# Optimization experiments

Measured on AMD Instinct MI355X. Metric: run time of the kernel, lower is better.

Reference implementation:

```python
import jax, jax.numpy as jnp
import numpy as np

# dims
A, T, K, H, NH, F, L = 64, 50, 6, 128, 8, 60, 512
M = A * T * K          # 19200 mode nodes (layout: agent, time, mode)
AT = A * T             # 3200 agent-timestep nodes
NL = 10                # GA layers: t2m,l2m,m2m_h,m2m_a,m2m_s,t2n,l2n,n2n_h,n2n_a,n2n_s
FF = 4 * H
E = 150000


def _ln(x, g, b):
    mu = x.mean(-1, keepdims=True)
    var = jnp.mean((x - mu) ** 2, axis=-1, keepdims=True)
    return (x - mu) * jax.lax.rsqrt(var + 1e-5) * g + b


def _mlp(x, W1, b1, W2, b2):
    return jax.nn.relu(x @ W1 + b1) @ W2 + b2


def _edge_emb(attr, i, eW1, eb1, eW2, eb2):
    # pad raw edge features to width 5 so all embed MLPs share a stacked param layout
    x = jnp.pad(attr, ((0, 0), (0, 5 - attr.shape[-1])))
    return jax.nn.relu(x @ eW1[i] + eb1[i]) @ eW2[i] + eb2[i]


def _segment_softmax(scores, dst, n):
    smax = jax.ops.segment_max(scores, dst, num_segments=n)
    smax = jnp.where(jnp.isfinite(smax), smax, 0.0)
    ex = jnp.exp(scores - smax[dst])
    den = jax.ops.segment_sum(ex, dst, num_segments=n)
    return ex / (den[dst] + 1e-9)


def _graph_attention(i, x_src, x_dst, ei, edge_emb, p):
    (Wq, Wk, Wv, Wo, Wke, Wve, g1, b1, g2, b2, fW1, fb1, fW2, fb2) = p
    src, dst = ei[0], ei[1]
    dh = H // NH
    n_dst = x_dst.shape[0]
    xd = _ln(x_dst, g1[i], b1[i])
    xs = _ln(x_src, g1[i], b1[i])
    q = (xd @ Wq[i]).reshape(n_dst, NH, dh)
    k = (xs @ Wk[i])[src]            # gather per-edge keys  [E,H]
    v = (xs @ Wv[i])[src]
    if edge_emb is not None:
        k = k + edge_emb @ Wke[i]
        v = v + edge_emb @ Wve[i]
    k = k.reshape(-1, NH, dh)
    v = v.reshape(-1, NH, dh)
    scores = jnp.sum(q[dst] * k, axis=-1) / np.sqrt(dh)   # [E,NH]
    attn = _segment_softmax(scores, dst, n_dst)
    agg = jax.ops.segment_sum(attn[..., None] * v, dst, num_segments=n_dst)
    x = x_dst + agg.reshape(n_dst, H) @ Wo[i]
    h = _ln(x, g2[i], b2[i])
    return x + _mlp(h, fW1[i], fb1[i], fW2[i], fb2[i])


def _forward(a_input, l_embs, mode_tokens,
             emb_W1, emb_b1, emb_W2, emb_b2,
             ga_Wq, ga_Wk, ga_Wv, ga_Wo, ga_Wke, ga_Wve,
             ga_g1, ga_b1, ga_g2, ga_b2, ga_fW1, ga_fb1, ga_fW2, ga_fb2,
             tp_W1, tp_b1, tp_W2, tp_b2,
             pa_W1, pa_b1, pa_W2, pa_b2,
             tr_W1, tr_b1, tr_W2, tr_b2,
             t2m_attr, l2m_attr, m2m_h_attr, m2m_a_attr,
             t2m_ei, l2m_ei, m2m_h_ei, m2m_a_ei, m2m_s_ei):
    ga = (ga_Wq, ga_Wk, ga_Wv, ga_Wo, ga_Wke, ga_Wve,
          ga_g1, ga_b1, ga_g2, ga_b2, ga_fW1, ga_fb1, ga_fW2, ga_fb2)
    # agent embedding: TwoLayerMLP on [vel_len, vel_theta, length, width, type]
    a_embs = (jax.nn.relu(a_input @ emb_W1[0] + emb_b1[0]) @ emb_W2[0] + emb_b2[0]).reshape(AT, H)
    # mode tokens broadcast over (agent, time)
    m = jnp.broadcast_to(mode_tokens, (A, T, K, H)).reshape(M, H)
    # edge-attr embeddings (gather-compute pattern)
    t2m_e = _edge_emb(t2m_attr, 1, emb_W1, emb_b1, emb_W2, emb_b2)
    l2m_e = _edge_emb(l2m_attr, 2, emb_W1, emb_b1, emb_W2, emb_b2)
    m2m_h_e = _edge_emb(m2m_h_attr, 3, emb_W1, emb_b1, emb_W2, emb_b2)
    m2m_a_e = _edge_emb(m2m_a_attr, 4, emb_W1, emb_b1, emb_W2, emb_b2)
    # proposal stage
    m = _graph_attention(0, a_embs, m, t2m_ei, t2m_e, ga)
    m = _graph_attention(1, l_embs, m, l2m_ei, l2m_e, ga)
    m = _graph_attention(2, m, m, m2m_h_ei, m2m_h_e, ga)
    m = _graph_attention(3, m, m, m2m_a_ei, m2m_a_e, ga)
    m = _graph_attention(4, m, m, m2m_s_ei, None, ga)
    m_last = m.reshape(A, T, K, H)[:, -1]                 # [A,K,H]
    proposal = _mlp(m_last, tp_W1, tp_b1, tp_W2, tp_b2)   # [A,K,2F]
    anchor = _mlp(proposal, pa_W1, pa_b1, pa_W2, pa_b2)   # [A,K,H]
    # refinement stage on anchor-conditioned mode nodes
    n = (m.reshape(A, T, K, H) + anchor[:, None]).reshape(M, H)
    n = _graph_attention(5, a_embs, n, t2m_ei, t2m_e, ga)
    n = _graph_attention(6, l_embs, n, l2m_ei, l2m_e, ga)
    n = _graph_attention(7, n, n, m2m_h_ei, m2m_h_e, ga)
    n = _graph_attention(8, n, n, m2m_a_ei, m2m_a_e, ga)
    n = _graph_attention(9, n, n, m2m_s_ei, None, ga)
    n_last = n.reshape(A, T, K, H)[:, -1]
    refine = proposal + _mlp(n_last, tr_W1, tr_b1, tr_W2, tr_b2)
    return jnp.stack([proposal, refine])                  # [2,A,K,2F]


def setup_inputs() -> dict:
    key = jax.random.key(0)
    ks = list(jax.random.split(key, 64))
    it = iter(ks)
    nx = lambda: next(it)
    p = lambda *s: 0.02 * jax.random.normal(nx(), s, dtype=jnp.float32)
    inp = {}
    inp['a_input'] = jax.random.normal(nx(), (A, T, 5), dtype=jnp.float32)
    inp['l_embs'] = jax.random.normal(nx(), (L, H), dtype=jnp.float32)
    inp['mode_tokens'] = p(K, H)
    # stacked edge/feature embed MLPs: 0:a,1:t2m,2:l2m,3:m2m_h,4:m2m_a
    inp['emb_W1'] = p(5, 5, H); inp['emb_b1'] = jnp.zeros((5, H), jnp.float32)
    inp['emb_W2'] = p(5, H, H); inp['emb_b2'] = jnp.zeros((5, H), jnp.float32)
    # stacked GraphAttention params
    for nm in ['ga_Wq', 'ga_Wk', 'ga_Wv', 'ga_Wo', 'ga_Wke', 'ga_Wve']:
        inp[nm] = p(NL, H, H)
    inp['ga_g1'] = jnp.ones((NL, H), jnp.float32); inp['ga_b1'] = jnp.zeros((NL, H), jnp.float32)
    inp['ga_g2'] = jnp.ones((NL, H), jnp.float32); inp['ga_b2'] = jnp.zeros((NL, H), jnp.float32)
    inp['ga_fW1'] = p(NL, H, FF); inp['ga_fb1'] = jnp.zeros((NL, FF), jnp.float32)
    inp['ga_fW2'] = p(NL, FF, H); inp['ga_fb2'] = jnp.zeros((NL, H), jnp.float32)
    # heads
    inp['tp_W1'] = p(H, H); inp['tp_b1'] = jnp.zeros((H,), jnp.float32)
    inp['tp_W2'] = p(H, 2 * F); inp['tp_b2'] = jnp.zeros((2 * F,), jnp.float32)
    inp['pa_W1'] = p(2 * F, H); inp['pa_b1'] = jnp.zeros((H,), jnp.float32)
    inp['pa_W2'] = p(H, H); inp['pa_b2'] = jnp.zeros((H,), jnp.float32)
    inp['tr_W1'] = p(H, H); inp['tr_b1'] = jnp.zeros((H,), jnp.float32)
    inp['tr_W2'] = p(H, 2 * F); inp['tr_b2'] = jnp.zeros((2 * F,), jnp.float32)
    # raw edge features
    inp['t2m_attr'] = jax.random.normal(nx(), (E, 4), dtype=jnp.float32)
    inp['l2m_attr'] = jax.random.normal(nx(), (E, 3), dtype=jnp.float32)
    inp['m2m_h_attr'] = jax.random.normal(nx(), (E, 4), dtype=jnp.float32)
    inp['m2m_a_attr'] = jax.random.normal(nx(), (E, 3), dtype=jnp.float32)
    # edge indices (src row range differs per graph)
    ri = lambda hi: jax.random.randint(nx(), (E,), 0, hi, dtype=jnp.int32)
    inp['t2m_ei'] = jnp.stack([ri(AT), ri(M)])
    inp['l2m_ei'] = jnp.stack([ri(L), ri(M)])
    inp['m2m_h_ei'] = jnp.stack([ri(M), ri(M)])
    inp['m2m_a_ei'] = jnp.stack([ri(M), ri(M)])
    inp['m2m_s_ei'] = jnp.stack([ri(M), ri(M)])
    return inp


def reference(a_input, l_embs, mode_tokens,
              emb_W1, emb_b1, emb_W2, emb_b2,
              ga_Wq, ga_Wk, ga_Wv, ga_Wo, ga_Wke, ga_Wve,
              ga_g1, ga_b1, ga_g2, ga_b2, ga_fW1, ga_fb1, ga_fW2, ga_fb2,
              tp_W1, tp_b1, tp_W2, tp_b2,
              pa_W1, pa_b1, pa_W2, pa_b2,
              tr_W1, tr_b1, tr_W2, tr_b2,
              t2m_attr, l2m_attr, m2m_h_attr, m2m_a_attr,
              t2m_ei, l2m_ei, m2m_h_ei, m2m_a_ei, m2m_s_ei):
    return _forward(a_input, l_embs, mode_tokens,
                    emb_W1, emb_b1, emb_W2, emb_b2,
                    ga_Wq, ga_Wk, ga_Wv, ga_Wo, ga_Wke, ga_Wve,
                    ga_g1, ga_b1, ga_g2, ga_b2, ga_fW1, ga_fb1, ga_fW2, ga_fb2,
                    tp_W1, tp_b1, tp_W2, tp_b2,
                    pa_W1, pa_b1, pa_W2, pa_b2,
                    tr_W1, tr_b1, tr_W2, tr_b2,
                    t2m_attr, l2m_attr, m2m_h_attr, m2m_a_attr,
                    t2m_ei, l2m_ei, m2m_h_ei, m2m_a_ei, m2m_s_ei)
```

## Files before the change

kernel.cpp:

```cpp
#include <hip/hip_runtime.h>
#include <hip/hip_bf16.h>
#include <math.h>

#define DEV __device__ __forceinline__

typedef __attribute__((ext_vector_type(4))) float floatx4;
typedef __attribute__((ext_vector_type(8))) __bf16 bf16x8;

static constexpr int A_ = 64, T_ = 50, K_ = 6, H_ = 128, NH_ = 8, F_ = 60, L_ = 512;
static constexpr int M_  = A_ * T_ * K_;
static constexpr int AT_ = A_ * T_;
static constexpr int FF_ = 4 * H_;
static constexpr int NL_ = 10;
static constexpr int P2F = 2 * F_;
static constexpr int AK_ = A_ * K_;
static constexpr size_t WLAY = 196608;

DEV ushort f2bh(float f) {
    unsigned u = __float_as_uint(f);
    unsigned r = u + 0x7FFFu + ((u >> 16) & 1u);
    return (ushort)(r >> 16);
}
DEV float bh2f(ushort h) { return __uint_as_float(((unsigned)h) << 16); }

__global__ __launch_bounds__(256) void ln_kernel(const float* __restrict__ x,
                                                 const float* __restrict__ g,
                                                 const float* __restrict__ b,
                                                 float* __restrict__ y, int n) {
    int row = blockIdx.x * 4 + (threadIdx.x >> 6);
    int lane = threadIdx.x & 63;
    if (row >= n) return;
    const float* xr = x + (size_t)row * H_;
    float v0 = xr[lane], v1 = xr[lane + 64];
    float s = v0 + v1;
    for (int m = 32; m >= 1; m >>= 1) s += __shfl_xor(s, m, 64);
    float mu = s * (1.f / 128.f);
    float d0 = v0 - mu, d1 = v1 - mu;
    float vs = d0 * d0 + d1 * d1;
    for (int m = 32; m >= 1; m >>= 1) vs += __shfl_xor(vs, m, 64);
    float rs = rsqrtf(vs * (1.f / 128.f) + 1e-5f);
    float* yr = y + (size_t)row * H_;
    yr[lane]      = d0 * rs * g[lane] + b[lane];
    yr[lane + 64] = d1 * rs * g[lane + 64] + b[lane + 64];
}

template <int ACT, bool RES>
__global__ __launch_bounds__(256) void mgemm(const float* __restrict__ X,
                                             const ushort* __restrict__ Wh,
                                             const ushort* __restrict__ Wl,
                                             const float* __restrict__ bias,
                                             const float* __restrict__ res,
                                             float* __restrict__ Y,
                                             int n, int Kd, int C) {
    __shared__ ushort lds[4 * 8192];
    ushort* Xh  = lds;
    ushort* Xl  = lds + 8192;
    ushort* Wsh = lds + 16384;
    ushort* Wsl = lds + 24576;
    int row0 = blockIdx.x * 128, col0 = blockIdx.y * 128;
    int tid = threadIdx.x;
    int lane = tid & 63, wid = tid >> 6;
    int rbase = (wid >> 1) * 64, cbase = (wid & 1) * 64;
    int lrow = lane & 15, lk = lane >> 4;
    floatx4 acc[4][4];
#pragma unroll
    for (int a = 0; a < 4; a++)
#pragma unroll
        for (int b2 = 0; b2 < 4; b2++) acc[a][b2] = floatx4{0.f, 0.f, 0.f, 0.f};

    for (int k0 = 0; k0 < Kd; k0 += 64) {
#pragma unroll
        for (int i = 0; i < 8; i++) {
            int idx = tid + i * 256;
            int r = idx >> 4, kc = idx & 15;
            float4 v = *(const float4*)(X + (size_t)(row0 + r) * Kd + k0 + kc * 4);
            ushort h0 = f2bh(v.x), h1 = f2bh(v.y), h2 = f2bh(v.z), h3 = f2bh(v.w);
            ushort l0 = f2bh(v.x - bh2f(h0)), l1 = f2bh(v.y - bh2f(h1)),
                   l2 = f2bh(v.z - bh2f(h2)), l3 = f2bh(v.w - bh2f(h3));
            int base = (r << 6) + (((kc >> 1) ^ (r & 7)) << 3) + ((kc & 1) << 2);
            *(ushort4*)(Xh + base) = make_ushort4(h0, h1, h2, h3);
            *(ushort4*)(Xl + base) = make_ushort4(l0, l1, l2, l3);
        }
#pragma unroll
        for (int i = 0; i < 4; i++) {
            int idx = tid + i * 256;
            int c = idx >> 3, ch = idx & 7;
            int base = (c << 6) + ((ch ^ (c & 7)) << 3);
            size_t go = (size_t)(col0 + c) * Kd + k0 + ch * 8;
            *(float4*)(Wsh + base) = *(const float4*)(Wh + go);
            *(float4*)(Wsl + base) = *(const float4*)(Wl + go);
        }
        __syncthreads();
#pragma unroll
        for (int kk = 0; kk < 2; kk++) {
            int ch = kk * 4 + lk;
            bf16x8 xh[4], xl[4], wh[4], wl[4];
#pragma unroll
            for (int s = 0; s < 4; s++) {
                int r = rbase + s * 16 + lrow;
                int xoff = (r << 6) + ((ch ^ (r & 7)) << 3);
                xh[s] = *(const bf16x8*)(Xh + xoff);
                xl[s] = *(const bf16x8*)(Xl + xoff);
                int c = cbase + s * 16 + lrow;
                int woff = (c << 6) + ((ch ^ (c & 7)) << 3);
                wh[s] = *(const bf16x8*)(Wsh + woff);
                wl[s] = *(const bf16x8*)(Wsl + woff);
            }
#pragma unroll
            for (int sr = 0; sr < 4; sr++)
#pragma unroll
                for (int sc = 0; sc < 4; sc++) {
                    acc[sr][sc] = __builtin_amdgcn_mfma_f32_16x16x32_bf16(wh[sc], xh[sr], acc[sr][sc], 0, 0, 0);
                    acc[sr][sc] = __builtin_amdgcn_mfma_f32_16x16x32_bf16(wl[sc], xh[sr], acc[sr][sc], 0, 0, 0);
                    acc[sr][sc] = __builtin_amdgcn_mfma_f32_16x16x32_bf16(wh[sc], xl[sr], acc[sr][sc], 0, 0, 0);
                }
        }
        __syncthreads();
    }
#pragma unroll
    for (int sr = 0; sr < 4; sr++) {
        int row = row0 + rbase + sr * 16 + lrow;
#pragma unroll
        for (int sc = 0; sc < 4; sc++) {
            int col = col0 + cbase + sc * 16 + lk * 4;
            size_t o = (size_t)row * C + col;
            float4 v = make_float4(acc[sr][sc][0], acc[sr][sc][1],
                                   acc[sr][sc][2], acc[sr][sc][3]);
            if (bias) { float4 bv = *(const float4*)(bias + col);
                        v.x += bv.x; v.y += bv.y; v.z += bv.z; v.w += bv.w; }
            if (ACT == 1) { v.x = fmaxf(v.x, 0.f); v.y = fmaxf(v.y, 0.f);
                            v.z = fmaxf(v.z, 0.f); v.w = fmaxf(v.w, 0.f); }
            if (RES) { float4 rv = *(const float4*)(res + o);
                       v.x += rv.x; v.y += rv.y; v.z += rv.z; v.w += rv.w; }
            *(float4*)(Y + o) = v;
        }
    }
}

__global__ __launch_bounds__(256) void prep_w(const float* __restrict__ Wq,
                                              const float* __restrict__ Wk,
                                              const float* __restrict__ Wv,
                                              const float* __restrict__ Wo,
                                              const float* __restrict__ fW1,
                                              const float* __restrict__ fW2,
                                              ushort* __restrict__ oh,
                                              ushort* __restrict__ ol) {
    int l = blockIdx.y, t = blockIdx.x;
    const float* src; int K, C, tiles_c; size_t obase;
    if (t < 64) {
        int mi = t >> 4; t &= 15;
        src = (mi == 0 ? Wq : mi == 1 ? Wk : mi == 2 ? Wv : Wo) + (size_t)l * 16384;
        K = 128; C = 128; tiles_c = 4; obase = (size_t)l * WLAY + (size_t)mi * 16384;
    } else if (t < 128) {
        t -= 64; src = fW1 + (size_t)l * 65536;
        K = 128; C = 512; tiles_c = 16; obase = (size_t)l * WLAY + 65536;
    } else {
        t -= 128; src = fW2 + (size_t)l * 65536;
        K = 512; C = 128; tiles_c = 4; obase = (size_t)l * WLAY + 131072;
    }
    int tc = t % tiles_c, tk = t / tiles_c;
    __shared__ float tile[32][33];
    int tx = threadIdx.x & 31, ty = threadIdx.x >> 5;
#pragma unroll
    for (int i = 0; i < 4; i++) {
        int k = tk * 32 + ty + i * 8;
        tile[ty + i * 8][tx] = src[(size_t)k * C + tc * 32 + tx];
    }
    __syncthreads();
#pragma unroll
    for (int i = 0; i < 4; i++) {
        int c = tc * 32 + ty + i * 8;
        float v = tile[tx][ty + i * 8];
        ushort h = f2bh(v);
        ushort lo = f2bh(v - bh2f(h));
        size_t o = obase + (size_t)c * K + tk * 32 + tx;
        oh[o] = h; ol[o] = lo;
    }
}

template <int ACT, bool RES>
__global__ void small_gemm(const float* __restrict__ X, const float* __restrict__ W,
                           const float* __restrict__ bias, const float* __restrict__ res,
                           float* __restrict__ Y, int n, int Kd, int C) {
    int idx = blockIdx.x * 256 + threadIdx.x;
    if (idx >= n * C) return;
    int row = idx / C, c = idx - row * C;
    float a = bias ? bias[c] : 0.f;
    const float* xr = X + (size_t)row * Kd;
    for (int k = 0; k < Kd; k++) a = fmaf(xr[k], W[(size_t)k * C + c], a);
    if (ACT == 1) a = fmaxf(a, 0.f);
    if (RES) a += res[idx];
    Y[idx] = a;
}

__global__ __launch_bounds__(256) void combine_fast(const float* __restrict__ eW2,
                                                    const float* __restrict__ Wke,
                                                    const float* __restrict__ Wve,
                                                    float* __restrict__ cW) {
    __shared__ float Xs[128 * 36];
    __shared__ float Ws[32 * 128];
    int x = blockIdx.x;
    int li = x & 7, kv = x >> 3;
    int l = li < 4 ? li : li + 1;
    int g = (li & 3) + 1;
    const float* E2 = eW2 + (size_t)g * 16384;
    const float* Wp = (kv ? Wve : Wke) + (size_t)l * 16384;
    float* out = cW + (size_t)l * 32768 + kv * 128;
    int tid = threadIdx.x;
    int tc = tid & 15, tr = tid >> 4;
    int cA = tc * 4, rA = tr * 4;
    float acc[8][8] = {};
    for (int j0 = 0; j0 < 128; j0 += 32) {
#pragma unroll
        for (int i = 0; i < 4; i++) {
            int idx = tid + i * 256;
            int r = idx >> 3, jc = idx & 7;
            *(float4*)(Xs + r * 36 + jc * 4) =
                *(const float4*)(E2 + (size_t)r * 128 + j0 + jc * 4);
        }
#pragma unroll
        for (int i = 0; i < 4; i++) {
            int idx = tid + i * 256;
            int cc = idx & 31, jj = idx >> 5;
            *(float4*)(Ws + jj * 128 + cc * 4) =
                *(const float4*)(Wp + (size_t)(j0 + jj) * 128 + cc * 4);
        }
        __syncthreads();
#pragma unroll 8
        for (int jj = 0; jj < 32; jj++) {
            float4 w0 = *(const float4*)(Ws + jj * 128 + cA);
            float4 w1 = *(const float4*)(Ws + jj * 128 + cA + 64);
            float xr[8];
#pragma unroll
            for (int i2 = 0; i2 < 4; i2++) {
                xr[i2]     = Xs[(rA + i2) * 36 + jj];
                xr[4 + i2] = Xs[(rA + i2 + 64) * 36 + jj];
            }
#pragma unroll
            for (int i2 = 0; i2 < 8; i2++) {
                float xv = xr[i2];
                acc[i2][0] = fmaf(xv, w0.x, acc[i2][0]);
                acc[i2][1] = fmaf(xv, w0.y, acc[i2][1]);
                acc[i2][2] = fmaf(xv, w0.z, acc[i2][2]);
                acc[i2][3] = fmaf(xv, w0.w, acc[i2][3]);
                acc[i2][4] = fmaf(xv, w1.x, acc[i2][4]);
                acc[i2][5] = fmaf(xv, w1.y, acc[i2][5]);
                acc[i2][6] = fmaf(xv, w1.z, acc[i2][6]);
                acc[i2][7] = fmaf(xv, w1.w, acc[i2][7]);
            }
        }
        __syncthreads();
    }
#pragma unroll
    for (int i = 0; i < 8; i++) {
        int r = (i < 4) ? (rA + i) : (rA + i + 60);
#pragma unroll
        for (int chh = 0; chh < 2; chh++) {
            int c = cA + chh * 64;
            *(float4*)(out + (size_t)r * 256 + c) =
                make_float4(acc[i][chh * 4 + 0], acc[i][chh * 4 + 1],
                            acc[i][chh * 4 + 2], acc[i][chh * 4 + 3]);
        }
    }
}
__global__ void combine_bias(const float* __restrict__ eb2,
                             const float* __restrict__ Wke,
                             const float* __restrict__ Wve,
                             float* __restrict__ cb) {
    int x = blockIdx.x;
    int li = x & 7, kv = x >> 3;
    int l = li < 4 ? li : li + 1;
    int g = (li & 3) + 1;
    const float* Wp = (kv ? Wve : Wke) + (size_t)l * 16384;
    const float* eb = eb2 + g * 128;
    int cc = threadIdx.x;
    float a = 0.f;
    for (int j = 0; j < 128; j++) a = fmaf(eb[j], Wp[(size_t)j * 128 + cc], a);
    cb[l * 256 + kv * 128 + cc] = a;
}

__global__ void zero_i32(int* __restrict__ p, int n) {
    int i = blockIdx.x * 256 + threadIdx.x;
    if (i < n) p[i] = 0;
}
__global__ void hist_kernel(const int* __restrict__ dst, int E, int* __restrict__ deg) {
    int e = blockIdx.x * 256 + threadIdx.x;
    if (e < E) atomicAdd(&deg[dst[e]], 1);
}
__global__ __launch_bounds__(256) void exscan5(const int* __restrict__ deg0,
                                               int* __restrict__ off0,
                                               int* __restrict__ cursor0, int n) {
    int g = blockIdx.x;
    const int* deg = deg0 + (size_t)g * n;
    int* off = off0 + (size_t)g * (n + 1);
    int* cursor = cursor0 + (size_t)g * n;
    __shared__ int wsum[4];
    __shared__ int carry;
    int tid = threadIdx.x, lane = tid & 63, w = tid >> 6;
    if (tid == 0) carry = 0;
    __syncthreads();
    for (int base = 0; base < n; base += 256) {
        int v = (base + tid < n) ? deg[base + tid] : 0;
        int incl = v;
        for (int d = 1; d < 64; d <<= 1) {
            int t = __shfl_up(incl, d, 64);
            if (lane >= d) incl += t;
        }
        if (lane == 63) wsum[w] = incl;
        __syncthreads();
        int woff = 0;
        for (int i = 0; i < w; i++) woff += wsum[i];
        int total = wsum[0] + wsum[1] + wsum[2] + wsum[3];
        int excl = carry + woff + incl - v;
        if (base + tid < n) { off[base + tid] = excl; cursor[base + tid] = excl; }
        __syncthreads();
        if (tid == 0) carry += total;
        __syncthreads();
    }
    if (threadIdx.x == 0) off[n] = carry;
}
__global__ void scatter_kernel(const int* __restrict__ dst, int E,
                               int* __restrict__ cursor, int* __restrict__ eids) {
    int e = blockIdx.x * 256 + threadIdx.x;
    if (e < E) { int p = atomicAdd(&cursor[dst[e]], 1); eids[p] = e; }
}
__global__ void sort_edges(const int* __restrict__ eid, const int* __restrict__ srcArr,
                           const float* __restrict__ attr, int aw, int E,
                           int* __restrict__ esrc, float4* __restrict__ eattr) {
    int pos = blockIdx.x * 256 + threadIdx.x;
    if (pos >= E) return;
    int e = eid[pos];
    esrc[pos] = srcArr[e];
    if (attr) {
        float4 v;
        v.x = attr[(size_t)e * aw + 0];
        v.y = attr[(size_t)e * aw + 1];
        v.z = (aw > 2) ? attr[(size_t)e * aw + 2] : 0.f;
        v.w = (aw > 3) ? attr[(size_t)e * aw + 3] : 0.f;
        eattr[pos] = v;
    }
}

__global__ __launch_bounds__(256) void prep_g(const float* __restrict__ q,
                                              const float* __restrict__ cWl,
                                              const float* __restrict__ cbl,
                                              ushort* __restrict__ g,
                                              float* __restrict__ sb) {
    __shared__ float qs[8 * 132];
    int tid = threadIdx.x;
    int cp = tid & 127, hb = (tid >> 7) * 4;
    float ck[64];
    {
        const float* csrc = cWl + (size_t)cp * 256 + hb * 16;
#pragma unroll
        for (int t4 = 0; t4 < 16; t4++) {
            float4 v = *(const float4*)(csrc + t4 * 4);
            ck[t4 * 4 + 0] = v.x; ck[t4 * 4 + 1] = v.y;
            ck[t4 * 4 + 2] = v.z; ck[t4 * 4 + 3] = v.w;
        }
    }
    int d0 = blockIdx.x * 8;
    {
        int dl = tid >> 5, col = (tid & 31) * 4;
        *(float4*)(qs + dl * 132 + col) = *(const float4*)(q + (size_t)(d0 + dl) * 128 + col);
    }
    __syncthreads();
#pragma unroll
    for (int dl = 0; dl < 8; dl++) {
        const float* qr = qs + dl * 132 + hb * 16;
        float a0 = 0.f, a1 = 0.f, a2 = 0.f, a3 = 0.f;
#pragma unroll
        for (int t = 0; t < 16; t++) {
            a0 = fmaf(ck[t],      qr[t],      a0);
            a1 = fmaf(ck[16 + t], qr[16 + t], a1);
            a2 = fmaf(ck[32 + t], qr[32 + t], a2);
            a3 = fmaf(ck[48 + t], qr[48 + t], a3);
        }
        ushort4 o = make_ushort4(f2bh(a0 * 0.25f), f2bh(a1 * 0.25f),
                                 f2bh(a2 * 0.25f), f2bh(a3 * 0.25f));
        *(ushort4*)(g + (size_t)(d0 + dl) * 1024 + cp * 8 + hb) = o;
    }
    if (tid < 64) {
        int dl = tid >> 3, h = tid & 7;
        const float* qr = qs + dl * 132 + h * 16;
        const float* cbr = cbl + h * 16;
        float a = 0.f;
#pragma unroll
        for (int t = 0; t < 16; t++) a = fmaf(cbr[t], qr[t], a);
        sb[(d0 + dl) * 8 + h] = a * 0.25f;
    }
}

__global__ __launch_bounds__(256) void attn_fact(const int* __restrict__ off,
                                                 const int* __restrict__ esrc,
                                                 const float4* __restrict__ eattr,
                                                 const ushort* __restrict__ g,
                                                 const float* __restrict__ sb,
                                                 const float* __restrict__ eW1,
                                                 const float* __restrict__ eb1,
                                                 const float* __restrict__ kx,
                                                 const float* __restrict__ vx,
                                                 const float* __restrict__ q,
                                                 ushort* __restrict__ hsum,
                                                 float* __restrict__ vxacc,
                                                 float* __restrict__ den) {
    __shared__ float lds[4 * 144];
    int w = threadIdx.x >> 6, l = threadIdx.x & 63;
    int i = l & 15, hlo = l >> 4;
    float* hw = lds + w * 144;
    int d = blockIdx.x * 4 + w;
    int beg = off[d], end = off[d + 1];
    float q0 = q[(size_t)d * 128 + l] * 0.25f;
    float q1 = q[(size_t)d * 128 + 64 + l] * 0.25f;
    float gA[8], gB[8];
#pragma unroll
    for (int j = 0; j < 8; j++) {
        gA[j] = bh2f(g[(size_t)d * 1024 + (j * 16 + i) * 8 + hlo]);
        gB[j] = bh2f(g[(size_t)d * 1024 + (j * 16 + i) * 8 + hlo + 4]);
    }
    float sbA = sb[d * 8 + hlo], sbB = sb[d * 8 + 4 + hlo];
    float w1a[4], w1b[4];
#pragma unroll
    for (int j = 0; j < 4; j++) { w1a[j] = eW1[j * 128 + l]; w1b[j] = eW1[j * 128 + 64 + l]; }
    float ebA = eb1[l], ebB = eb1[64 + l];
    float mA = -INFINITY, mB = -INFINITY, dnA = 0.f, dnB = 0.f;
    float accL[8] = {}, accH[8] = {};
    float va0 = 0.f, va1 = 0.f;
    float4 aC = make_float4(0.f, 0.f, 0.f, 0.f);
    float k0C = 0.f, k1C = 0.f, v0C = 0.f, v1C = 0.f;
    if (beg < end) {
        int s0 = esrc[beg]; aC = eattr[beg];
        const float* kxr = kx + (size_t)s0 * 128;
        const float* vxr = vx + (size_t)s0 * 128;
        k0C = kxr[l]; k1C = kxr[64 + l];
        v0C = vxr[l]; v1C = vxr[64 + l];
    }
    for (int pos = beg; pos < end; pos++) {
        float4 at = aC;
        float k0 = k0C, k1 = k1C, v0 = v0C, v1 = v1C;
        if (pos + 1 < end) {
            int sN = esrc[pos + 1]; aC = eattr[pos + 1];
            const float* kxr = kx + (size_t)sN * 128;
            const float* vxr = vx + (size_t)sN * 128;
            k0C = kxr[l]; k1C = kxr[64 + l];
            v0C = vxr[l]; v1C = vxr[64 + l];
        }
        float h0 = fmaxf(ebA + at.x * w1a[0] + at.y * w1a[1] + at.z * w1a[2] + at.w * w1a[3], 0.f);
        float h1 = fmaxf(ebB + at.x * w1b[0] + at.y * w1b[1] + at.z * w1b[2] + at.w * w1b[3], 0.f);
        hw[l] = h0; hw[64 + l] = h1;
        __builtin_amdgcn_wave_barrier();
        float pA = q0 * k0, pB = q1 * k1;
#pragma unroll
        for (int j = 0; j < 8; j++) {
            float hv = hw[j * 16 + i];
            pA = fmaf(hv, gA[j], pA);
            pB = fmaf(hv, gB[j], pB);
        }
#pragma unroll
        for (int msk = 1; msk < 16; msk <<= 1) {
            pA += __shfl_xor(pA, msk, 64);
            pB += __shfl_xor(pB, msk, 64);
        }
        pA += sbA; pB += sbB;
        float nmA = fmaxf(mA, pA), nmB = fmaxf(mB, pB);
        float cA = __expf(mA - nmA), cB = __expf(mB - nmB);
        float wA = __expf(pA - nmA), wB = __expf(pB - nmB);
        mA = nmA; mB = nmB;
        dnA = dnA * cA + wA; dnB = dnB * cB + wB;
        va0 = va0 * cA + wA * v0; va1 = va1 * cB + wB * v1;
        if (i == 0) {
            hw[128 + hlo] = wA; hw[132 + hlo] = wB;
            hw[136 + hlo] = cA; hw[140 + hlo] = cB;
        }
        __builtin_amdgcn_wave_barrier();
        float4 wv0 = *(float4*)(hw + 128), wv1 = *(float4*)(hw + 132);
        float4 cv0 = *(float4*)(hw + 136), cv1 = *(float4*)(hw + 140);
        accL[0] = fmaf(accL[0], cv0.x, wv0.x * h0); accH[0] = fmaf(accH[0], cv0.x, wv0.x * h1);
        accL[1] = fmaf(accL[1], cv0.y, wv0.y * h0); accH[1] = fmaf(accH[1], cv0.y, wv0.y * h1);
        accL[2] = fmaf(accL[2], cv0.z, wv0.z * h0); accH[2] = fmaf(accH[2], cv0.z, wv0.z * h1);
        accL[3] = fmaf(accL[3], cv0.w, wv0.w * h0); accH[3] = fmaf(accH[3], cv0.w, wv0.w * h1);
        accL[4] = fmaf(accL[4], cv1.x, wv1.x * h0); accH[4] = fmaf(accH[4], cv1.x, wv1.x * h1);
        accL[5] = fmaf(accL[5], cv1.y, wv1.y * h0); accH[5] = fmaf(accH[5], cv1.y, wv1.y * h1);
        accL[6] = fmaf(accL[6], cv1.z, wv1.z * h0); accH[6] = fmaf(accH[6], cv1.z, wv1.z * h1);
        accL[7] = fmaf(accL[7], cv1.w, wv1.w * h0); accH[7] = fmaf(accH[7], cv1.w, wv1.w * h1);
    }
#pragma unroll
    for (int h = 0; h < 8; h++) {
        hsum[(size_t)d * 1024 + h * 128 + l]      = f2bh(accL[h]);
        hsum[(size_t)d * 1024 + h * 128 + 64 + l] = f2bh(accH[h]);
    }
    vxacc[(size_t)d * 128 + l] = va0;
    vxacc[(size_t)d * 128 + 64 + l] = va1;
    if (i == 0) { den[d * 8 + hlo] = dnA; den[d * 8 + 4 + hlo] = dnB; }
}

__global__ __launch_bounds__(256) void attn_plain(const int* __restrict__ off,
                                                  const int* __restrict__ esrc,
                                                  const float* __restrict__ kx,
                                                  const float* __restrict__ vx,
                                                  const float* __restrict__ q,
                                                  float* __restrict__ agg) {
    int w = threadIdx.x >> 6, lane = threadIdx.x & 63;
    int d = blockIdx.x * 4 + w;
    int beg = off[d], end = off[d + 1];
    float q0 = q[(size_t)d * 128 + lane] * 0.25f;
    float q1 = q[(size_t)d * 128 + 64 + lane] * 0.25f;
    float m0 = -INFINITY, m1 = -INFINITY;
    float den0 = 0.f, den1 = 0.f, acc0 = 0.f, acc1 = 0.f;
    float k0C = 0.f, k1C = 0.f, v0C = 0.f, v1C = 0.f;
    if (beg < end) {
        int s0 = esrc[beg];
        const float* kxr = kx + (size_t)s0 * 128;
        const float* vxr = vx + (size_t)s0 * 128;
        k0C = kxr[lane]; k1C = kxr[64 + lane];
        v0C = vxr[lane]; v1C = vxr[64 + lane];
    }
    for (int pos = beg; pos < end; pos++) {
        float k0 = k0C, k1 = k1C, v0 = v0C, v1 = v1C;
        if (pos + 1 < end) {
            int sN = esrc[pos + 1];
            const float* kxr = kx + (size_t)sN * 128;
            const float* vxr = vx + (size_t)sN * 128;
            k0C = kxr[lane]; k1C = kxr[64 + lane];
            v0C = vxr[lane]; v1C = vxr[64 + lane];
        }
        float p0 = q0 * k0, p1 = q1 * k1;
#pragma unroll
        for (int msk = 1; msk < 16; msk <<= 1) {
            p0 += __shfl_xor(p0, msk, 64);
            p1 += __shfl_xor(p1, msk, 64);
        }
        float nm0 = fmaxf(m0, p0), nm1 = fmaxf(m1, p1);
        float c0 = __expf(m0 - nm0), c1 = __expf(m1 - nm1);
        float e0 = __expf(p0 - nm0), e1 = __expf(p1 - nm1);
        acc0 = acc0 * c0 + e0 * v0; den0 = den0 * c0 + e0;
        acc1 = acc1 * c1 + e1 * v1; den1 = den1 * c1 + e1;
        m0 = nm0; m1 = nm1;
    }
    agg[(size_t)d * 128 + lane]      = acc0 / (den0 + 1e-9f);
    agg[(size_t)d * 128 + 64 + lane] = acc1 / (den1 + 1e-9f);
}

static constexpr int HST_ = 1092;
__global__ __launch_bounds__(256) void agg_fin(const ushort* __restrict__ hsum,
                                               const float* __restrict__ vxacc,
                                               const float* __restrict__ den,
                                               const float* __restrict__ cWl,
                                               const float* __restrict__ cbl,
                                               float* __restrict__ agg) {
    __shared__ float Cvs[128 * 128];
    __shared__ float hstage[8 * HST_];
    __shared__ float dens[64];
    int tid = threadIdx.x;
    {
        int cp = tid >> 1, cb0 = (tid & 1) * 64;
#pragma unroll
        for (int kq = 0; kq < 16; kq++)
            *(float4*)(Cvs + cp * 128 + cb0 + kq * 4) =
                *(const float4*)(cWl + (size_t)cp * 256 + 128 + cb0 + kq * 4);
    }
    int j = tid & 31, dsel = tid >> 5;
    int c4 = j * 4, h = j >> 2;
    float4 cvb = *(const float4*)(cbl + 128 + c4);
    for (int d0 = blockIdx.x * 8; d0 < M_; d0 += gridDim.x * 8) {
        __syncthreads();
        int r = tid * 4;
#pragma unroll
        for (int k = 0; k < 8; k++) {
            ushort4 u = *(const ushort4*)(hsum + (size_t)(d0 + k) * 1024 + r);
            *(float4*)(hstage + k * HST_ + (r >> 7) * 136 + (r & 127)) =
                make_float4(bh2f(u.x), bh2f(u.y), bh2f(u.z), bh2f(u.w));
        }
        if (tid < 64) dens[tid] = den[d0 * 8 + tid];
        __syncthreads();
        int d = d0 + dsel;
        float dn = dens[dsel * 8 + h];
        float inv = 1.f / (dn + 1e-9f);
        float cf = dn * inv;
        float a0 = 0.f, a1 = 0.f, a2 = 0.f, a3 = 0.f;
        const float* hrow = hstage + dsel * HST_ + h * 136;
#pragma unroll 4
        for (int cpp = 0; cpp < 128; cpp++) {
            float hs = hrow[cpp];
            float4 cv = *(float4*)(Cvs + cpp * 128 + c4);
            a0 = fmaf(hs, cv.x, a0); a1 = fmaf(hs, cv.y, a1);
            a2 = fmaf(hs, cv.z, a2); a3 = fmaf(hs, cv.w, a3);
        }
        float4 vv = *(const float4*)(vxacc + (size_t)d * 128 + c4);
        float4 o;
        o.x = (vv.x + a0) * inv + cvb.x * cf;
        o.y = (vv.y + a1) * inv + cvb.y * cf;
        o.z = (vv.z + a2) * inv + cvb.z * cf;
        o.w = (vv.w + a3) * inv + cvb.w * cf;
        *(float4*)(agg + (size_t)d * 128 + c4) = o;
    }
}

__global__ void mode_init(float* __restrict__ m, const float* __restrict__ mt) {
    int idx = blockIdx.x * 256 + threadIdx.x;
    if (idx >= M_ * H_) return;
    int node = idx >> 7, c = idx & 127;
    m[idx] = mt[(node % K_) * H_ + c];
}
__global__ void extract_last(const float* __restrict__ m, float* __restrict__ out) {
    int idx = blockIdx.x * 256 + threadIdx.x;
    if (idx >= AK_ * H_) return;
    int row = idx >> 7, c = idx & 127;
    int a = row / K_, k = row - a * K_;
    int node = (a * T_ + (T_ - 1)) * K_ + k;
    out[idx] = m[(size_t)node * H_ + c];
}
__global__ void add_anchor(float* __restrict__ m, const float* __restrict__ anchor) {
    int idx = blockIdx.x * 256 + threadIdx.x;
    if (idx >= M_ * H_) return;
    int node = idx >> 7, c = idx & 127;
    int a = node / (T_ * K_), k = node % K_;
    m[idx] += anchor[(size_t)(a * K_ + k) * H_ + c];
}

extern "C" void kernel_launch(void* const* d_in, const int* in_sizes, int n_in,
                              void* d_out, int out_size, void* d_ws, size_t ws_size,
                              hipStream_t stream) {
    const float* a_input     = (const float*)d_in[0];
    const float* l_embs      = (const float*)d_in[1];
    const float* mode_tokens = (const float*)d_in[2];
    const float* emb_W1 = (const float*)d_in[3];
    const float* emb_b1 = (const float*)d_in[4];
    const float* emb_W2 = (const float*)d_in[5];
    const float* emb_b2 = (const float*)d_in[6];
    const float* ga_Wq  = (const float*)d_in[7];
    const float* ga_Wk  = (const float*)d_in[8];
    const float* ga_Wv  = (const float*)d_in[9];
    const float* ga_Wo  = (const float*)d_in[10];
    const float* ga_Wke = (const float*)d_in[11];
    const float* ga_Wve = (const float*)d_in[12];
    const float* ga_g1  = (const float*)d_in[13];
    const float* ga_b1  = (const float*)d_in[14];
    const float* ga_g2  = (const float*)d_in[15];
    const float* ga_b2  = (const float*)d_in[16];
    const float* ga_fW1 = (const float*)d_in[17];
    const float* ga_fb1 = (const float*)d_in[18];
    const float* ga_fW2 = (const float*)d_in[19];
    const float* ga_fb2 = (const float*)d_in[20];
    const float* tp_W1 = (const float*)d_in[21];
    const float* tp_b1 = (const float*)d_in[22];
    const float* tp_W2 = (const float*)d_in[23];
    const float* tp_b2 = (const float*)d_in[24];
    const float* pa_W1 = (const float*)d_in[25];
    const float* pa_b1 = (const float*)d_in[26];
    const float* pa_W2 = (const float*)d_in[27];
    const float* pa_b2 = (const float*)d_in[28];
    const float* tr_W1 = (const float*)d_in[29];
    const float* tr_b1 = (const float*)d_in[30];
    const float* tr_W2 = (const float*)d_in[31];
    const float* tr_b2 = (const float*)d_in[32];
    const float* attrs[4] = { (const float*)d_in[33], (const float*)d_in[34],
                              (const float*)d_in[35], (const float*)d_in[36] };
    const int* eis[5] = { (const int*)d_in[37], (const int*)d_in[38], (const int*)d_in[39],
                          (const int*)d_in[40], (const int*)d_in[41] };
    int Es[5];
    int Emax = 0;
    for (int i = 0; i < 5; i++) { Es[i] = in_sizes[37 + i] / 2; if (Es[i] > Emax) Emax = Es[i]; }

    size_t off = 0;
    auto alloc = [&](size_t nbytes) -> char* {
        char* p = (char*)d_ws + off;
        off += ((nbytes + 255) / 256) * 256;
        return p;
    };
    float* cW     = (float*)alloc((size_t)NL_ * 128 * 256 * 4);
    float* cb     = (float*)alloc((size_t)NL_ * 256 * 4);
    ushort* wbh   = (ushort*)alloc((size_t)NL_ * WLAY * 2);
    ushort* wbl   = (ushort*)alloc((size_t)NL_ * WLAY * 2);
    float* a_embs = (float*)alloc((size_t)AT_ * H_ * 4);
    float* m      = (float*)alloc((size_t)M_ * H_ * 4);
    float* xd_ln  = (float*)alloc((size_t)M_ * H_ * 4);
    float* xs_ln  = (float*)alloc((size_t)AT_ * H_ * 4);
    float* q      = (float*)alloc((size_t)M_ * H_ * 4);
    float* kx     = (float*)alloc((size_t)M_ * H_ * 4);
    float* vx     = (float*)alloc((size_t)M_ * H_ * 4);
    float* agg    = (float*)alloc((size_t)M_ * H_ * 4);
    float* big    = (float*)alloc((size_t)M_ * FF_ * 4);
    ushort* gbuf  = (ushort*)alloc((size_t)M_ * 1024 * 2);
    ushort* hsumb = (ushort*)alloc((size_t)M_ * 1024 * 2);
    float* vxacc  = (float*)alloc((size_t)M_ * H_ * 4);
    float* den    = (float*)alloc((size_t)M_ * 8 * 4);
    float* sb     = (float*)alloc((size_t)M_ * 8 * 4);
    int* csr_off  = (int*)alloc((size_t)5 * (M_ + 1) * 4);
    int* csr_eid  = (int*)alloc((size_t)5 * Emax * 4);
    int* esrc     = (int*)alloc((size_t)5 * Emax * 4);
    float4* eattr = (float4*)alloc((size_t)4 * Emax * 16);
    int* deg5     = (int*)alloc((size_t)5 * M_ * 4);
    int* cursor5  = (int*)alloc((size_t)5 * M_ * 4);
    float* mlast  = (float*)alloc((size_t)AK_ * H_ * 4);
    float* hbuf   = (float*)alloc((size_t)AK_ * H_ * 4);
    float* anchor = (float*)alloc((size_t)AK_ * H_ * 4);
    (void)ws_size; (void)n_in;

    float* outp = (float*)d_out;

    zero_i32<<<(5 * M_ + 255) / 256, 256, 0, stream>>>(deg5, 5 * M_);
    for (int gI = 0; gI < 5; gI++)
        hist_kernel<<<(Es[gI] + 255) / 256, 256, 0, stream>>>(eis[gI] + Es[gI], Es[gI], deg5 + (size_t)gI * M_);
    exscan5<<<5, 256, 0, stream>>>(deg5, csr_off, cursor5, M_);
    for (int gI = 0; gI < 5; gI++)
        scatter_kernel<<<(Es[gI] + 255) / 256, 256, 0, stream>>>(eis[gI] + Es[gI], Es[gI],
            cursor5 + (size_t)gI * M_, csr_eid + (size_t)gI * Emax);
    for (int gI = 0; gI < 5; gI++) {
        int aw = (gI == 0 || gI == 2) ? 4 : (gI == 4 ? 0 : 3);
        sort_edges<<<(Es[gI] + 255) / 256, 256, 0, stream>>>(
            csr_eid + (size_t)gI * Emax, eis[gI], (gI < 4) ? attrs[gI] : nullptr, aw, Es[gI],
            esrc + (size_t)gI * Emax, eattr + (size_t)gI * Emax);
    }

    prep_w<<<dim3(192, 10), 256, 0, stream>>>(ga_Wq, ga_Wk, ga_Wv, ga_Wo, ga_fW1, ga_fW2, wbh, wbl);
    combine_fast<<<16, 256, 0, stream>>>(emb_W2, ga_Wke, ga_Wve, cW);
    combine_bias<<<16, 128, 0, stream>>>(emb_b2, ga_Wke, ga_Wve, cb);

    small_gemm<1, false><<<(AT_ * H_ + 255) / 256, 256, 0, stream>>>(a_input, emb_W1, emb_b1, nullptr, big, AT_, 5, H_);
    small_gemm<0, false><<<(AT_ * H_ + 255) / 256, 256, 0, stream>>>(big, emb_W2, emb_b2, nullptr, a_embs, AT_, H_, H_);
    mode_init<<<(M_ * H_ + 255) / 256, 256, 0, stream>>>(m, mode_tokens);

    struct Cfg { const float* srcX; int n_src; int gi; bool hasE; };
    Cfg cfgs[10] = {
        { a_embs, AT_, 0, true }, { l_embs, L_, 1, true },
        { nullptr, M_, 2, true }, { nullptr, M_, 3, true },
        { nullptr, M_, 4, false },
        { a_embs, AT_, 0, true }, { l_embs, L_, 1, true },
        { nullptr, M_, 2, true }, { nullptr, M_, 3, true },
        { nullptr, M_, 4, false },
    };

    for (int l = 0; l < 10; l++) {
        const Cfg& cf = cfgs[l];
        const int* offg = csr_off + cf.gi * (M_ + 1);
        const int* esrcg = esrc + (size_t)cf.gi * Emax;
        const float4* eattrg = eattr + (size_t)cf.gi * Emax;
        const float* g1 = ga_g1 + l * H_; const float* b1 = ga_b1 + l * H_;
        size_t wb = (size_t)l * WLAY;

        ln_kernel<<<M_ / 4, 256, 0, stream>>>(m, g1, b1, xd_ln, M_);
        mgemm<0, false><<<dim3(M_ / 128, 1), 256, 0, stream>>>(
            xd_ln, wbh + wb, wbl + wb, nullptr, nullptr, q, M_, 128, 128);
        const float* srcLN = xd_ln;
        if (cf.srcX) {
            ln_kernel<<<cf.n_src / 4, 256, 0, stream>>>(cf.srcX, g1, b1, xs_ln, cf.n_src);
            srcLN = xs_ln;
        }
        mgemm<0, false><<<dim3(cf.n_src / 128, 1), 256, 0, stream>>>(
            srcLN, wbh + wb + 16384, wbl + wb + 16384, nullptr, nullptr, kx, cf.n_src, 128, 128);
        mgemm<0, false><<<dim3(cf.n_src / 128, 1), 256, 0, stream>>>(
            srcLN, wbh + wb + 32768, wbl + wb + 32768, nullptr, nullptr, vx, cf.n_src, 128, 128);

        if (cf.hasE) {
            int gg = (l < 5) ? l + 1 : l - 4;
            const float* eW1g = emb_W1 + (size_t)gg * 5 * H_;
            const float* eb1g = emb_b1 + (size_t)gg * H_;
            prep_g<<<M_ / 8, 256, 0, stream>>>(q, cW + (size_t)l * 128 * 256, cb + l * 256, gbuf, sb);
            attn_fact<<<M_ / 4, 256, 0, stream>>>(offg, esrcg, eattrg, gbuf, sb, eW1g, eb1g,
                                                  kx, vx, q, hsumb, vxacc, den);
            agg_fin<<<256, 256, 0, stream>>>(hsumb, vxacc, den,
                                             cW + (size_t)l * 128 * 256, cb + l * 256, agg);
        } else {
            attn_plain<<<M_ / 4, 256, 0, stream>>>(offg, esrcg, kx, vx, q, agg);
        }

        mgemm<0, true><<<dim3(M_ / 128, 1), 256, 0, stream>>>(
            agg, wbh + wb + 49152, wbl + wb + 49152, nullptr, m, m, M_, 128, 128);
        ln_kernel<<<M_ / 4, 256, 0, stream>>>(m, ga_g2 + l * H_, ga_b2 + l * H_, xd_ln, M_);
        mgemm<1, false><<<dim3(M_ / 128, 4), 256, 0, stream>>>(
            xd_ln, wbh + wb + 65536, wbl + wb + 65536, ga_fb1 + l * FF_, nullptr, big, M_, 128, 512);
        mgemm<0, true><<<dim3(M_ / 128, 1), 256, 0, stream>>>(
            big, wbh + wb + 131072, wbl + wb + 131072, ga_fb2 + l * H_, m, m, M_, 512, 128);

        if (l == 4) {
            extract_last<<<(AK_ * H_ + 255) / 256, 256, 0, stream>>>(m, mlast);
            small_gemm<1, false><<<(AK_ * H_ + 255) / 256, 256, 0, stream>>>(mlast, tp_W1, tp_b1, nullptr, hbuf, AK_, H_, H_);
            small_gemm<0, false><<<(AK_ * P2F + 255) / 256, 256, 0, stream>>>(hbuf, tp_W2, tp_b2, nullptr, outp, AK_, H_, P2F);
            small_gemm<1, false><<<(AK_ * H_ + 255) / 256, 256, 0, stream>>>(outp, pa_W1, pa_b1, nullptr, hbuf, AK_, P2F, H_);
            small_gemm<0, false><<<(AK_ * H_ + 255) / 256, 256, 0, stream>>>(hbuf, pa_W2, pa_b2, nullptr, anchor, AK_, H_, H_);
            add_anchor<<<(M_ * H_ + 255) / 256, 256, 0, stream>>>(m, anchor);
        }
    }

    extract_last<<<(AK_ * H_ + 255) / 256, 256, 0, stream>>>(m, mlast);
    small_gemm<1, false><<<(AK_ * H_ + 255) / 256, 256, 0, stream>>>(mlast, tr_W1, tr_b1, nullptr, hbuf, AK_, H_, H_);
    small_gemm<0, true><<<(AK_ * P2F + 255) / 256, 256, 0, stream>>>(hbuf, tr_W2, tr_b2, outp, outp + AK_ * P2F, AK_, H_, P2F);
}
```

Measured before the change: 2.694 ms.

## Fuse Q/K/V projections into one GEMM and drop online-softmax max tracking

Merges the separate Q, K and V projection GEMMs into a single wide GEMM writing an interleaved qkv buffer, or Q plus a fused KV GEMM when source nodes differ. The attention kernels now read K and V from one strided row. The online softmax's running max and rescaling are removed, so raw exponentials are accumulated directly. This cuts launches, exp calls and per-edge rescale FMAs, but risks overflow if scores grow large, since the max subtraction no longer protects against it.

```diff
diff --git a/kernel.cpp b/kernel.cpp
--- a/kernel.cpp
+++ b/kernel.cpp
@@ -341,7 +341,7 @@
     }
 }
 
-__global__ __launch_bounds__(256) void prep_g(const float* __restrict__ q,
+__global__ __launch_bounds__(256) void prep_g(const float* __restrict__ qkv,
                                               const float* __restrict__ cWl,
                                               const float* __restrict__ cbl,
                                               ushort* __restrict__ g,
@@ -362,7 +362,7 @@
     int d0 = blockIdx.x * 8;
     {
         int dl = tid >> 5, col = (tid & 31) * 4;
-        *(float4*)(qs + dl * 132 + col) = *(const float4*)(q + (size_t)(d0 + dl) * 128 + col);
+        *(float4*)(qs + dl * 132 + col) = *(const float4*)(qkv + (size_t)(d0 + dl) * 384 + col);
     }
     __syncthreads();
 #pragma unroll
@@ -398,9 +398,8 @@
                                                  const float* __restrict__ sb,
                                                  const float* __restrict__ eW1,
                                                  const float* __restrict__ eb1,
-                                                 const float* __restrict__ kx,
-                                                 const float* __restrict__ vx,
-                                                 const float* __restrict__ q,
+                                                 const float* __restrict__ qkv,
+                                                 const float* __restrict__ kvp, int KS,
                                                  ushort* __restrict__ hsum,
                                                  float* __restrict__ vxacc,
                                                  float* __restrict__ den) {
@@ -410,8 +409,8 @@
     float* hw = lds + w * 144;
     int d = blockIdx.x * 4 + w;
     int beg = off[d], end = off[d + 1];
-    float q0 = q[(size_t)d * 128 + l] * 0.25f;
-    float q1 = q[(size_t)d * 128 + 64 + l] * 0.25f;
+    float q0 = qkv[(size_t)d * 384 + l] * 0.25f;
+    float q1 = qkv[(size_t)d * 384 + 64 + l] * 0.25f;
     float gA[8], gB[8];
 #pragma unroll
     for (int j = 0; j < 8; j++) {
@@ -423,27 +422,25 @@
 #pragma unroll
     for (int j = 0; j < 4; j++) { w1a[j] = eW1[j * 128 + l]; w1b[j] = eW1[j * 128 + 64 + l]; }
     float ebA = eb1[l], ebB = eb1[64 + l];
-    float mA = -INFINITY, mB = -INFINITY, dnA = 0.f, dnB = 0.f;
+    float dnA = 0.f, dnB = 0.f;
     float accL[8] = {}, accH[8] = {};
     float va0 = 0.f, va1 = 0.f;
     float4 aC = make_float4(0.f, 0.f, 0.f, 0.f);
     float k0C = 0.f, k1C = 0.f, v0C = 0.f, v1C = 0.f;
     if (beg < end) {
         int s0 = esrc[beg]; aC = eattr[beg];
-        const float* kxr = kx + (size_t)s0 * 128;
-        const float* vxr = vx + (size_t)s0 * 128;
-        k0C = kxr[l]; k1C = kxr[64 + l];
-        v0C = vxr[l]; v1C = vxr[64 + l];
+        const float* r = kvp + (size_t)s0 * KS;
+        k0C = r[l]; k1C = r[64 + l];
+        v0C = r[128 + l]; v1C = r[192 + l];
     }
     for (int pos = beg; pos < end; pos++) {
         float4 at = aC;
         float k0 = k0C, k1 = k1C, v0 = v0C, v1 = v1C;
         if (pos + 1 < end) {
             int sN = esrc[pos + 1]; aC = eattr[pos + 1];
-            const float* kxr = kx + (size_t)sN * 128;
-            const float* vxr = vx + (size_t)sN * 128;
-            k0C = kxr[l]; k1C = kxr[64 + l];
-            v0C = vxr[l]; v1C = vxr[64 + l];
+            const float* r = kvp + (size_t)sN * KS;
+            k0C = r[l]; k1C = r[64 + l];
+            v0C = r[128 + l]; v1C = r[192 + l];
         }
         float h0 = fmaxf(ebA + at.x * w1a[0] + at.y * w1a[1] + at.z * w1a[2] + at.w * w1a[3], 0.f);
         float h1 = fmaxf(ebB + at.x * w1b[0] + at.y * w1b[1] + at.z * w1b[2] + at.w * w1b[3], 0.f);
@@ -461,28 +458,23 @@
             pA += __shfl_xor(pA, msk, 64);
             pB += __shfl_xor(pB, msk, 64);
         }
-        pA += sbA; pB += sbB;
-        float nmA = fmaxf(mA, pA), nmB = fmaxf(mB, pB);
-        float cA = __expf(mA - nmA), cB = __expf(mB - nmB);
-        float wA = __expf(pA - nmA), wB = __expf(pB - nmB);
-        mA = nmA; mB = nmB;
-        dnA = dnA * cA + wA; dnB = dnB * cB + wB;
-        va0 = va0 * cA + wA * v0; va1 = va1 * cB + wB * v1;
-        if (i == 0) {
-            hw[128 + hlo] = wA; hw[132 + hlo] = wB;
-            hw[136 + hlo] = cA; hw[140 + hlo] = cB;
-        }
+        float wA = __expf(pA + sbA);
+        float wB = __expf(pB + sbB);
+        dnA += wA; dnB += wB;
+        va0 = fmaf(wA, v0, va0);
+        va1 = fmaf(wB, v1, va1);
+        if (i == 0) { hw[128 + hlo] = wA; hw[132 + hlo] = wB; }
         __builtin_amdgcn_wave_barrier();
-        float4 wv0 = *(float4*)(hw + 128), wv1 = *(float4*)(hw + 132);
-        float4 cv0 = *(float4*)(hw + 136), cv1 = *(float4*)(hw + 140);
-        accL[0] = fmaf(accL[0], cv0.x, wv0.x * h0); accH[0] = fmaf(accH[0], cv0.x, wv0.x * h1);
-        accL[1] = fmaf(accL[1], cv0.y, wv0.y * h0); accH[1] = fmaf(accH[1], cv0.y, wv0.y * h1);
-        accL[2] = fmaf(accL[2], cv0.z, wv0.z * h0); accH[2] = fmaf(accH[2], cv0.z, wv0.z * h1);
-        accL[3] = fmaf(accL[3], cv0.w, wv0.w * h0); accH[3] = fmaf(accH[3], cv0.w, wv0.w * h1);
-        accL[4] = fmaf(accL[4], cv1.x, wv1.x * h0); accH[4] = fmaf(accH[4], cv1.x, wv1.x * h1);
-        accL[5] = fmaf(accL[5], cv1.y, wv1.y * h0); accH[5] = fmaf(accH[5], cv1.y, wv1.y * h1);
-        accL[6] = fmaf(accL[6], cv1.z, wv1.z * h0); accH[6] = fmaf(accH[6], cv1.z, wv1.z * h1);
-        accL[7] = fmaf(accL[7], cv1.w, wv1.w * h0); accH[7] = fmaf(accH[7], cv1.w, wv1.w * h1);
+        float4 WA = *(float4*)(hw + 128), WB = *(float4*)(hw + 132);
+#pragma unroll
+        for (int j = 0; j < 4; j++) {
+            float wa = ((const float*)&WA)[j];
+            float wb = ((const float*)&WB)[j];
+            accL[j]     = fmaf(wa, h0, accL[j]);
+            accH[j]     = fmaf(wa, h1, accH[j]);
+            accL[4 + j] = fmaf(wb, h0, accL[4 + j]);
+            accH[4 + j] = fmaf(wb, h1, accH[4 + j]);
+        }
     }
 #pragma unroll
     for (int h = 0; h < 8; h++) {
@@ -496,33 +488,29 @@
 
 __global__ __launch_bounds__(256) void attn_plain(const int* __restrict__ off,
                                                   const int* __restrict__ esrc,
-                                                  const float* __restrict__ kx,
-                                                  const float* __restrict__ vx,
-                                                  const float* __restrict__ q,
+                                                  const float* __restrict__ qkv,
+                                                  const float* __restrict__ kvp, int KS,
                                                   float* __restrict__ agg) {
-    int w = threadIdx.x >> 6, lane = threadIdx.x & 63;
-    int d = blockIdx.x * 4 + w;
+    int lane = threadIdx.x & 63;
+    int d = blockIdx.x * 4 + (threadIdx.x >> 6);
     int beg = off[d], end = off[d + 1];
-    float q0 = q[(size_t)d * 128 + lane] * 0.25f;
-    float q1 = q[(size_t)d * 128 + 64 + lane] * 0.25f;
-    float m0 = -INFINITY, m1 = -INFINITY;
+    float q0 = qkv[(size_t)d * 384 + lane] * 0.25f;
+    float q1 = qkv[(size_t)d * 384 + 64 + lane] * 0.25f;
     float den0 = 0.f, den1 = 0.f, acc0 = 0.f, acc1 = 0.f;
     float k0C = 0.f, k1C = 0.f, v0C = 0.f, v1C = 0.f;
     if (beg < end) {
         int s0 = esrc[beg];
-        const float* kxr = kx + (size_t)s0 * 128;
-        const float* vxr = vx + (size_t)s0 * 128;
-        k0C = kxr[lane]; k1C = kxr[64 + lane];
-        v0C = vxr[lane]; v1C = vxr[64 + lane];
+        const float* r = kvp + (size_t)s0 * KS;
+        k0C = r[lane]; k1C = r[64 + lane];
+        v0C = r[128 + lane]; v1C = r[192 + lane];
     }
     for (int pos = beg; pos < end; pos++) {
         float k0 = k0C, k1 = k1C, v0 = v0C, v1 = v1C;
         if (pos + 1 < end) {
             int sN = esrc[pos + 1];
-            const float* kxr = kx + (size_t)sN * 128;
-            const float* vxr = vx + (size_t)sN * 128;
-            k0C = kxr[lane]; k1C = kxr[64 + lane];
-            v0C = vxr[lane]; v1C = vxr[64 + lane];
+            const float* r = kvp + (size_t)sN * KS;
+            k0C = r[lane]; k1C = r[64 + lane];
+            v0C = r[128 + lane]; v1C = r[192 + lane];
         }
         float p0 = q0 * k0, p1 = q1 * k1;
 #pragma unroll
@@ -530,12 +518,10 @@
             p0 += __shfl_xor(p0, msk, 64);
             p1 += __shfl_xor(p1, msk, 64);
         }
-        float nm0 = fmaxf(m0, p0), nm1 = fmaxf(m1, p1);
-        float c0 = __expf(m0 - nm0), c1 = __expf(m1 - nm1);
-        float e0 = __expf(p0 - nm0), e1 = __expf(p1 - nm1);
-        acc0 = acc0 * c0 + e0 * v0; den0 = den0 * c0 + e0;
-        acc1 = acc1 * c1 + e1 * v1; den1 = den1 * c1 + e1;
-        m0 = nm0; m1 = nm1;
+        float w0 = __expf(p0), w1 = __expf(p1);
+        den0 += w0; den1 += w1;
+        acc0 = fmaf(w0, v0, acc0);
+        acc1 = fmaf(w1, v1, acc1);
     }
     agg[(size_t)d * 128 + lane]      = acc0 / (den0 + 1e-9f);
     agg[(size_t)d * 128 + 64 + lane] = acc1 / (den1 + 1e-9f);
@@ -676,9 +662,8 @@
     float* m      = (float*)alloc((size_t)M_ * H_ * 4);
     float* xd_ln  = (float*)alloc((size_t)M_ * H_ * 4);
     float* xs_ln  = (float*)alloc((size_t)AT_ * H_ * 4);
-    float* q      = (float*)alloc((size_t)M_ * H_ * 4);
-    float* kx     = (float*)alloc((size_t)M_ * H_ * 4);
-    float* vx     = (float*)alloc((size_t)M_ * H_ * 4);
+    float* qkv    = (float*)alloc((size_t)M_ * 384 * 4);
+    float* kvs    = (float*)alloc((size_t)AT_ * 256 * 4);
     float* agg    = (float*)alloc((size_t)M_ * H_ * 4);
     float* big    = (float*)alloc((size_t)M_ * FF_ * 4);
     ushort* gbuf  = (ushort*)alloc((size_t)M_ * 1024 * 2);
@@ -740,29 +725,32 @@
         size_t wb = (size_t)l * WLAY;
 
         ln_kernel<<<M_ / 4, 256, 0, stream>>>(m, g1, b1, xd_ln, M_);
-        mgemm<0, false><<<dim3(M_ / 128, 1), 256, 0, stream>>>(
-            xd_ln, wbh + wb, wbl + wb, nullptr, nullptr, q, M_, 128, 128);
-        const float* srcLN = xd_ln;
+        const float* kvp;
+        int KS;
         if (cf.srcX) {
+            mgemm<0, false><<<dim3(M_ / 128, 1), 256, 0, stream>>>(
+                xd_ln, wbh + wb, wbl + wb, nullptr, nullptr, qkv, M_, 128, 384);
             ln_kernel<<<cf.n_src / 4, 256, 0, stream>>>(cf.srcX, g1, b1, xs_ln, cf.n_src);
-            srcLN = xs_ln;
-        }
-        mgemm<0, false><<<dim3(cf.n_src / 128, 1), 256, 0, stream>>>(
-            srcLN, wbh + wb + 16384, wbl + wb + 16384, nullptr, nullptr, kx, cf.n_src, 128, 128);
-        mgemm<0, false><<<dim3(cf.n_src / 128, 1), 256, 0, stream>>>(
-            srcLN, wbh + wb + 32768, wbl + wb + 32768, nullptr, nullptr, vx, cf.n_src, 128, 128);
+            mgemm<0, false><<<dim3(cf.n_src / 128, 2), 256, 0, stream>>>(
+                xs_ln, wbh + wb + 16384, wbl + wb + 16384, nullptr, nullptr, kvs, cf.n_src, 128, 256);
+            kvp = kvs; KS = 256;
+        } else {
+            mgemm<0, false><<<dim3(M_ / 128, 3), 256, 0, stream>>>(
+                xd_ln, wbh + wb, wbl + wb, nullptr, nullptr, qkv, M_, 128, 384);
+            kvp = qkv + 128; KS = 384;
+        }
 
         if (cf.hasE) {
             int gg = (l < 5) ? l + 1 : l - 4;
             const float* eW1g = emb_W1 + (size_t)gg * 5 * H_;
             const float* eb1g = emb_b1 + (size_t)gg * H_;
-            prep_g<<<M_ / 8, 256, 0, stream>>>(q, cW + (size_t)l * 128 * 256, cb + l * 256, gbuf, sb);
+            prep_g<<<M_ / 8, 256, 0, stream>>>(qkv, cW + (size_t)l * 128 * 256, cb + l * 256, gbuf, sb);
             attn_fact<<<M_ / 4, 256, 0, stream>>>(offg, esrcg, eattrg, gbuf, sb, eW1g, eb1g,
-                                                  kx, vx, q, hsumb, vxacc, den);
+                                                  qkv, kvp, KS, hsumb, vxacc, den);
             agg_fin<<<256, 256, 0, stream>>>(hsumb, vxacc, den,
                                              cW + (size_t)l * 128 * 256, cb + l * 256, agg);
         } else {
-            attn_plain<<<M_ / 4, 256, 0, stream>>>(offg, esrcg, kx, vx, q, agg);
+            attn_plain<<<M_ / 4, 256, 0, stream>>>(offg, esrcg, qkv, kvp, KS, agg);
         }
 
         mgemm<0, true><<<dim3(M_ / 128, 1), 256, 0, stream>>>(
```

Result: faster. 2.619 ms (-2.8%).
